# Performance work log

Measured on AMD Instinct MI355X. Metric: run time of the kernel, lower is better.

The kernel has to match this reference:

```python
import jax, jax.numpy as jnp
import numpy as np

TOTAL_WORDS = 10000
EMB = 100
SEQ = 80
UNITS = 64


def setup_inputs() -> dict:
    key = jax.random.key(0)
    ks = jax.random.split(key, 10)
    B = 16384
    tokens = jax.random.randint(ks[0], (B, SEQ), 0, TOTAL_WORDS, dtype=jnp.int32)
    s = 0.05
    emb = jax.random.normal(ks[1], (TOTAL_WORDS, EMB), jnp.float32) * s
    Wx0 = jax.random.normal(ks[2], (EMB, UNITS), jnp.float32) * s
    Wh0 = jax.random.normal(ks[3], (UNITS, UNITS), jnp.float32) * s
    b0 = jnp.zeros((UNITS,), jnp.float32)
    Wx1 = jax.random.normal(ks[4], (UNITS, UNITS), jnp.float32) * s
    Wh1 = jax.random.normal(ks[5], (UNITS, UNITS), jnp.float32) * s
    b1 = jnp.zeros((UNITS,), jnp.float32)
    Wout = jax.random.normal(ks[6], (UNITS, 1), jnp.float32) * s
    bout = jnp.zeros((1,), jnp.float32)
    return {"tokens": tokens, "emb": emb, "Wx0": Wx0, "Wh0": Wh0, "b0": b0,
            "Wx1": Wx1, "Wh1": Wh1, "b1": b1, "Wout": Wout, "bout": bout}


def reference(tokens, emb, Wx0, Wh0, b0, Wx1, Wh1, b1, Wout, bout):
    # Embedding lookup: [B, SEQ, EMB]
    x = emb[tokens]
    B = tokens.shape[0]
    # time-major for scan: [SEQ, B, EMB]
    xt = jnp.transpose(x, (1, 0, 2))
    h0 = jnp.zeros((B, UNITS), x.dtype)
    h1 = jnp.zeros((B, UNITS), x.dtype)

    def step(carry, x_t):
        h0, h1 = carry
        # SimpleRNNCell (inference, dropout inactive): h' = tanh(x Wx + h Wh + b)
        h0n = jnp.tanh(x_t @ Wx0 + h0 @ Wh0 + b0)
        h1n = jnp.tanh(h0n @ Wx1 + h1 @ Wh1 + b1)
        return (h0n, h1n), None

    (h0, h1), _ = jax.lax.scan(step, (h0, h1), xt)
    logits = h1 @ Wout + bout  # [B, 1]
    return jax.nn.sigmoid(logits)
```

## Files before the change

### kernel.cpp

```cpp
#include <hip/hip_runtime.h>

#define TOTAL_WORDS 10000
#define EMB 100
#define SEQ 80
#define UNITS 64
#define BATCH 16384


typedef _Float16 f16x4 __attribute__((ext_vector_type(4)));
typedef _Float16 f16x8 __attribute__((ext_vector_type(8)));
typedef _Float16 h2    __attribute__((ext_vector_type(2)));
typedef __fp16   fp16x2r __attribute__((ext_vector_type(2)));
typedef float    f32x4 __attribute__((ext_vector_type(4)));

__device__ __forceinline__ h2 pkcvt(float a, float b) {
    fp16x2r t = __builtin_amdgcn_cvt_pkrtz(a, b);
    h2 o; o[0] = (_Float16)t[0]; o[1] = (_Float16)t[1];
    return o;
}

__device__ __forceinline__ h2 tanh_h2(h2 x) {
    const _Float16 c3 = (_Float16)(-0.33333333f);
    const _Float16 c5 = (_Float16)(0.13333333f);
    h2 x2 = x * x;
    h2 p  = x2 * c5 + c3;
    h2 x3 = x2 * x;
    return x3 * p + x;
}

__device__ __forceinline__ f16x4 tanh_pack(f32x4 a) {
    h2 lo = tanh_h2(pkcvt(a[0], a[1]));
    h2 hi = tanh_h2(pkcvt(a[2], a[3]));
    f16x4 o;
    o[0] = lo[0]; o[1] = lo[1]; o[2] = hi[0]; o[3] = hi[1];
    return o;
}

__device__ __forceinline__ void lds_barrier() {
    asm volatile("s_waitcnt lgkmcnt(0)\n\ts_barrier" ::: "memory");
}

__global__ void prep_kernel(const float* __restrict__ emb,
                            const float* __restrict__ Wx0,
                            const float* __restrict__ b0,
                            const float* __restrict__ Wh0,
                            const float* __restrict__ Wx1,
                            const float* __restrict__ Wh1,
                            float* __restrict__ embW,
                            _Float16* __restrict__ wfrags) {
    int b = blockIdx.x;
    if (b < 250) {
        __shared__ float wx[EMB * UNITS];
        for (int i = threadIdx.x; i < EMB * UNITS; i += 256)
            wx[i] = Wx0[i];
        __syncthreads();
        const int u = threadIdx.x & 63;
        const int wvi = threadIdx.x >> 6;
        const int vbase = b * 40 + wvi * 10;
        const float bias = b0[u];
        float acc[10];
#pragma unroll
        for (int i = 0; i < 10; ++i) acc[i] = bias;
        const float* er = emb + vbase * EMB;
#pragma unroll 4
        for (int k = 0; k < EMB; ++k) {
            float wxv = wx[k * UNITS + u];
#pragma unroll
            for (int i = 0; i < 10; ++i)
                acc[i] = fmaf(er[i * EMB + k], wxv, acc[i]);
        }
#pragma unroll
        for (int i = 0; i < 10; ++i)
            embW[(vbase + i) * UNITS + u] = acc[i];
    } else {
        int e = (b - 250) * 256 + threadIdx.x;
        int mat = e >> 12;
        int ee = e & 4095;
        int f = ee >> 9;
        int mt = f >> 1, kf = f & 1;
        int rr = ee & 511;
        int l = rr >> 3, j = rr & 7;
        int k = kf * 32 + (l >> 4) * 8 + j;
        int col = mt * 16 + (l & 15);
        const float* W = (mat == 0) ? Wh0 : (mat == 1) ? Wx1 : Wh1;
        wfrags[e] = (_Float16)W[k * UNITS + col];
    }
}

#define RNN_STEP(EA, EB, T4)                                                  \
    {                                                                         \
        f32x4 a0 = EA, a1 = EB;               \
        f32x4 c0 = b1v0, c1 = b1v1;                  \
        a0 = __builtin_amdgcn_mfma_f32_16x16x32_f16(w0[0][0], h0f0, a0,0,0,0);\
        a1 = __builtin_amdgcn_mfma_f32_16x16x32_f16(w0[1][0], h0f0, a1,0,0,0);\
        c0 = __builtin_amdgcn_mfma_f32_16x16x32_f16(wh[0][0], h1f0, c0,0,0,0);\
        c1 = __builtin_amdgcn_mfma_f32_16x16x32_f16(wh[1][0], h1f0, c1,0,0,0);\
        a0 = __builtin_amdgcn_mfma_f32_16x16x32_f16(w0[0][1], h0f1, a0,0,0,0);\
        a1 = __builtin_amdgcn_mfma_f32_16x16x32_f16(w0[1][1], h0f1, a1,0,0,0);\
        c0 = __builtin_amdgcn_mfma_f32_16x16x32_f16(wh[0][1], h1f1, c0,0,0,0);\
        c1 = __builtin_amdgcn_mfma_f32_16x16x32_f16(wh[1][1], h1f1, c1,0,0,0);\
        EA = embWv[(T4) * 16 + (2 * p) * 4 + q];          \
        EB = embWv[(T4) * 16 + (2 * p + 1) * 4 + q];                          \
        {                                                                     \
            f16x4 n0 = tanh_pack(a0), n1 = tanh_pack(a1);                     \
            *(uint2*)&hbuf0[r][(2 * p) * 16 + 4 * q] = *(const uint2*)&n0;    \
            *(uint2*)&hbuf0[r][(2 * p + 1) * 16 + 4 * q] = *(const uint2*)&n1;\
        }                                                                     \
        lds_barrier();                                                        \
        h0f0 = *(const f16x8*)&hbuf0[r][8 * q];                               \
        h0f1 = *(const f16x8*)&hbuf0[r][32 + 8 * q];                          \
        c0 = __builtin_amdgcn_mfma_f32_16x16x32_f16(wx[0][0], h0f0, c0,0,0,0);\
        c1 = __builtin_amdgcn_mfma_f32_16x16x32_f16(wx[1][0], h0f0, c1,0,0,0);\
        c0 = __builtin_amdgcn_mfma_f32_16x16x32_f16(wx[0][1], h0f1, c0,0,0,0);\
        c1 = __builtin_amdgcn_mfma_f32_16x16x32_f16(wx[1][1], h0f1, c1,0,0,0);\
        {                                                                     \
            f16x4 n0 = tanh_pack(c0), n1 = tanh_pack(c1);                     \
            *(uint2*)&hbuf1[r][(2 * p) * 16 + 4 * q] = *(const uint2*)&n0;    \
            *(uint2*)&hbuf1[r][(2 * p + 1) * 16 + 4 * q] = *(const uint2*)&n1;\
        }                                                                     \
        lds_barrier();                                                        \
        h1f0 = *(const f16x8*)&hbuf1[r][8 * q];                               \
        h1f1 = *(const f16x8*)&hbuf1[r][32 + 8 * q];                          \
    }

__global__ __launch_bounds__(128, 2) void rnn_mfma_kernel(
    const int*      __restrict__ tokens,
    const float*    __restrict__ embW,
    const _Float16* __restrict__ wfrags,
    const float*    __restrict__ b1,
    const float*    __restrict__ Wout,
    const float*    __restrict__ bout,
    float*          __restrict__ out) {
    const int tid = threadIdx.x;
    const int p   = tid >> 6;
    const int l   = tid & 63;
    const int r   = l & 15;
    const int q   = l >> 4;
    const int row0 = blockIdx.x * 16;

    __shared__ __align__(16) _Float16 hbuf0[16][72];
    __shared__ __align__(16) _Float16 hbuf1[16][72];

    const f16x8* wf8 = (const f16x8*)wfrags;
    f16x8 w0[2][2], wx[2][2], wh[2][2];
#pragma unroll
    for (int j = 0; j < 2; ++j)
#pragma unroll
        for (int kf = 0; kf < 2; ++kf) {
            int mt = 2 * p + j;
            w0[j][kf] = wf8[(mt * 2 + kf) * 64 + l];
            wx[j][kf] = wf8[(8 + mt * 2 + kf) * 64 + l];
            wh[j][kf] = wf8[(16 + mt * 2 + kf) * 64 + l];
        }

    const f32x4 b1v0 = ((const f32x4*)b1)[(2 * p) * 4 + q];
    const f32x4 b1v1 = ((const f32x4*)b1)[(2 * p + 1) * 4 + q];

    f16x8 h0f0, h0f1, h1f0, h1f1;
#pragma unroll
    for (int j = 0; j < 8; ++j) {
        h0f0[j] = (_Float16)0.0f; h0f1[j] = (_Float16)0.0f;
        h1f0[j] = (_Float16)0.0f; h1f1[j] = (_Float16)0.0f;
    }

    const f32x4* embWv = (const f32x4*)embW;
    const int tokbase = (row0 + r) * SEQ;

    int4 tk0 = *(const int4*)&tokens[tokbase];
    int4 tk  = *(const int4*)&tokens[tokbase + 4];
    f32x4 e0a = embWv[tk0.x * 16 + (2 * p) * 4 + q];
    f32x4 e0b = embWv[tk0.x * 16 + (2 * p + 1) * 4 + q];
    f32x4 e1a = embWv[tk0.y * 16 + (2 * p) * 4 + q];
    f32x4 e1b = embWv[tk0.y * 16 + (2 * p + 1) * 4 + q];
    f32x4 e2a = embWv[tk0.z * 16 + (2 * p) * 4 + q];
    f32x4 e2b = embWv[tk0.z * 16 + (2 * p + 1) * 4 + q];
    f32x4 e3a = embWv[tk0.w * 16 + (2 * p) * 4 + q];
    f32x4 e3b = embWv[tk0.w * 16 + (2 * p + 1) * 4 + q];

    for (int k = 0; k < SEQ / 4; ++k) {
        int off = (4 * k + 8 <= SEQ - 4) ? (4 * k + 8) : (SEQ - 4);
        int4 tkC = *(const int4*)&tokens[tokbase + off];

        RNN_STEP(e0a, e0b, tk.x)
        RNN_STEP(e1a, e1b, tk.y)
        RNN_STEP(e2a, e2b, tk.z)
        RNN_STEP(e3a, e3b, tk.w)

        tk = tkC;
    }

    if (p == 0) {
        f32x4 wo0 = ((const f32x4*)Wout)[2 * q];
        f32x4 wo1 = ((const f32x4*)Wout)[2 * q + 1];
        f32x4 wo2 = ((const f32x4*)Wout)[8 + 2 * q];
        f32x4 wo3 = ((const f32x4*)Wout)[8 + 2 * q + 1];
        float accv = 0.0f;
#pragma unroll
        for (int j = 0; j < 4; ++j) {
            accv = fmaf((float)h1f0[j],     wo0[j], accv);
            accv = fmaf((float)h1f0[4 + j], wo1[j], accv);
            accv = fmaf((float)h1f1[j],     wo2[j], accv);
            accv = fmaf((float)h1f1[4 + j], wo3[j], accv);
        }
        accv += __shfl_down(accv, 16);
        accv += __shfl_down(accv, 32);
        if (l < 16) {
            float z = accv + bout[0];
            out[row0 + r] = 1.0f / (1.0f + __expf(-z));
        }
    }
}

extern "C" void kernel_launch(void* const* d_in, const int* in_sizes, int n_in,
                              void* d_out, int out_size, void* d_ws, size_t ws_size,
                              hipStream_t stream) {
    const int*   tokens = (const int*)d_in[0];
    const float* emb    = (const float*)d_in[1];
    const float* Wx0    = (const float*)d_in[2];
    const float* Wh0    = (const float*)d_in[3];
    const float* b0     = (const float*)d_in[4];
    const float* Wx1    = (const float*)d_in[5];
    const float* Wh1    = (const float*)d_in[6];
    const float* b1     = (const float*)d_in[7];
    const float* Wout   = (const float*)d_in[8];
    const float* bout   = (const float*)d_in[9];
    float* out = (float*)d_out;

    float* embW = (float*)d_ws;
    _Float16* wfrags =
        (_Float16*)((char*)d_ws + (size_t)TOTAL_WORDS * UNITS * 4);

    prep_kernel<<<298, 256, 0, stream>>>(emb, Wx0, b0, Wh0, Wx1, Wh1,
                                         embW, wfrags);
    rnn_mfma_kernel<<<BATCH / 16, 128, 0, stream>>>(tokens, embW, wfrags,
                                                    b1, Wout, bout, out);
}
```

Before: 130.7 us.

## Split RNN units across four waves and process two 16-row tiles per block

Each block now has four waves that each own one 16-unit M tile, and handles 32 batch rows as two independent 16-row tiles instead of one. Every wave issues two independent MFMA chains per substep, one per row tile, so fewer weight fragments stay resident and each wave has more independent work to hide MFMA and tanh latency. The embedding prefetch distance drops from four steps to two, and the barriers now synchronise four waves instead of two, so barrier cost and exposed gather latency may rise.

Result: slower. 134.3 us (+2.7%).

```diff
diff --git a/kernel.cpp b/kernel.cpp
--- a/kernel.cpp
+++ b/kernel.cpp
@@ -39,6 +39,8 @@
 __device__ __forceinline__ void lds_barrier() {
     asm volatile("s_waitcnt lgkmcnt(0)\n\ts_barrier" ::: "memory");
 }
+
+#define M32(W, H, C) __builtin_amdgcn_mfma_f32_16x16x32_f16((W), (H), (C), 0, 0, 0)
 
 __global__ void prep_kernel(const float* __restrict__ emb,
                             const float* __restrict__ Wx0,
@@ -87,43 +89,44 @@
     }
 }
 
-#define RNN_STEP(EA, EB, T4)                                                  \
+#define SUBSTEP(E0, E1, T20, T21)                                             \
     {                                                                         \
-        f32x4 a0 = EA, a1 = EB;               \
-        f32x4 c0 = b1v0, c1 = b1v1;                  \
-        a0 = __builtin_amdgcn_mfma_f32_16x16x32_f16(w0[0][0], h0f0, a0,0,0,0);\
-        a1 = __builtin_amdgcn_mfma_f32_16x16x32_f16(w0[1][0], h0f0, a1,0,0,0);\
-        c0 = __builtin_amdgcn_mfma_f32_16x16x32_f16(wh[0][0], h1f0, c0,0,0,0);\
-        c1 = __builtin_amdgcn_mfma_f32_16x16x32_f16(wh[1][0], h1f0, c1,0,0,0);\
-        a0 = __builtin_amdgcn_mfma_f32_16x16x32_f16(w0[0][1], h0f1, a0,0,0,0);\
-        a1 = __builtin_amdgcn_mfma_f32_16x16x32_f16(w0[1][1], h0f1, a1,0,0,0);\
-        c0 = __builtin_amdgcn_mfma_f32_16x16x32_f16(wh[0][1], h1f1, c0,0,0,0);\
-        c1 = __builtin_amdgcn_mfma_f32_16x16x32_f16(wh[1][1], h1f1, c1,0,0,0);\
-        EA = embWv[(T4) * 16 + (2 * p) * 4 + q];          \
-        EB = embWv[(T4) * 16 + (2 * p + 1) * 4 + q];                          \
+        f32x4 a0 = E0, a1 = E1;                                               \
+        f32x4 c0 = b1v, c1 = b1v;                                             \
+                          \
+        a0 = M32(w0f[0], h0A0, a0);  a1 = M32(w0f[0], h0A1, a1);              \
+        c0 = M32(whf[0], h1A0, c0);  c1 = M32(whf[0], h1A1, c1);              \
+        a0 = M32(w0f[1], h0B0, a0);  a1 = M32(w0f[1], h0B1, a1);              \
+        c0 = M32(whf[1], h1B0, c0);  c1 = M32(whf[1], h1B1, c1);              \
         {                                                                     \
             f16x4 n0 = tanh_pack(a0), n1 = tanh_pack(a1);                     \
-            *(uint2*)&hbuf0[r][(2 * p) * 16 + 4 * q] = *(const uint2*)&n0;    \
-            *(uint2*)&hbuf0[r][(2 * p + 1) * 16 + 4 * q] = *(const uint2*)&n1;\
+            *(uint2*)&hbuf0[0][r][p * 16 + 4 * q] = *(const uint2*)&n0;       \
+            *(uint2*)&hbuf0[1][r][p * 16 + 4 * q] = *(const uint2*)&n1;       \
         }                                                                     \
         lds_barrier();                                                        \
-        h0f0 = *(const f16x8*)&hbuf0[r][8 * q];                               \
-        h0f1 = *(const f16x8*)&hbuf0[r][32 + 8 * q];                          \
-        c0 = __builtin_amdgcn_mfma_f32_16x16x32_f16(wx[0][0], h0f0, c0,0,0,0);\
-        c1 = __builtin_amdgcn_mfma_f32_16x16x32_f16(wx[1][0], h0f0, c1,0,0,0);\
-        c0 = __builtin_amdgcn_mfma_f32_16x16x32_f16(wx[0][1], h0f1, c0,0,0,0);\
-        c1 = __builtin_amdgcn_mfma_f32_16x16x32_f16(wx[1][1], h0f1, c1,0,0,0);\
+        h0A0 = *(const f16x8*)&hbuf0[0][r][8 * q];                            \
+        h0B0 = *(const f16x8*)&hbuf0[0][r][32 + 8 * q];                       \
+        h0A1 = *(const f16x8*)&hbuf0[1][r][8 * q];                            \
+        h0B1 = *(const f16x8*)&hbuf0[1][r][32 + 8 * q];                       \
+                      \
+        E0 = embWv[(T20) * 16 + p * 4 + q];                                   \
+        E1 = embWv[(T21) * 16 + p * 4 + q];                                   \
+                            \
+        c0 = M32(wxf[0], h0A0, c0);  c1 = M32(wxf[0], h0A1, c1);              \
+        c0 = M32(wxf[1], h0B0, c0);  c1 = M32(wxf[1], h0B1, c1);              \
         {                                                                     \
             f16x4 n0 = tanh_pack(c0), n1 = tanh_pack(c1);                     \
-            *(uint2*)&hbuf1[r][(2 * p) * 16 + 4 * q] = *(const uint2*)&n0;    \
-            *(uint2*)&hbuf1[r][(2 * p + 1) * 16 + 4 * q] = *(const uint2*)&n1;\
+            *(uint2*)&hbuf1[0][r][p * 16 + 4 * q] = *(const uint2*)&n0;       \
+            *(uint2*)&hbuf1[1][r][p * 16 + 4 * q] = *(const uint2*)&n1;       \
         }                                                                     \
         lds_barrier();                                                        \
-        h1f0 = *(const f16x8*)&hbuf1[r][8 * q];                               \
-        h1f1 = *(const f16x8*)&hbuf1[r][32 + 8 * q];                          \
-    }
-
-__global__ __launch_bounds__(128, 2) void rnn_mfma_kernel(
+        h1A0 = *(const f16x8*)&hbuf1[0][r][8 * q];                            \
+        h1B0 = *(const f16x8*)&hbuf1[0][r][32 + 8 * q];                       \
+        h1A1 = *(const f16x8*)&hbuf1[1][r][8 * q];                            \
+        h1B1 = *(const f16x8*)&hbuf1[1][r][32 + 8 * q];                       \
+    }
+
+__global__ __launch_bounds__(256, 2) void rnn_mfma_kernel(
     const int*      __restrict__ tokens,
     const float*    __restrict__ embW,
     const _Float16* __restrict__ wfrags,
@@ -136,57 +139,53 @@
     const int l   = tid & 63;
     const int r   = l & 15;
     const int q   = l >> 4;
-    const int row0 = blockIdx.x * 16;
-
-    __shared__ __align__(16) _Float16 hbuf0[16][72];
-    __shared__ __align__(16) _Float16 hbuf1[16][72];
+    const int row0 = blockIdx.x * 32;
+
+    __shared__ __align__(16) _Float16 hbuf0[2][16][72];
+    __shared__ __align__(16) _Float16 hbuf1[2][16][72];
 
     const f16x8* wf8 = (const f16x8*)wfrags;
-    f16x8 w0[2][2], wx[2][2], wh[2][2];
-#pragma unroll
-    for (int j = 0; j < 2; ++j)
-#pragma unroll
-        for (int kf = 0; kf < 2; ++kf) {
-            int mt = 2 * p + j;
-            w0[j][kf] = wf8[(mt * 2 + kf) * 64 + l];
-            wx[j][kf] = wf8[(8 + mt * 2 + kf) * 64 + l];
-            wh[j][kf] = wf8[(16 + mt * 2 + kf) * 64 + l];
-        }
-
-    const f32x4 b1v0 = ((const f32x4*)b1)[(2 * p) * 4 + q];
-    const f32x4 b1v1 = ((const f32x4*)b1)[(2 * p + 1) * 4 + q];
-
-    f16x8 h0f0, h0f1, h1f0, h1f1;
+    f16x8 w0f[2], wxf[2], whf[2];
+#pragma unroll
+    for (int kf = 0; kf < 2; ++kf) {
+        w0f[kf] = wf8[(p * 2 + kf) * 64 + l];
+        wxf[kf] = wf8[(8 + p * 2 + kf) * 64 + l];
+        whf[kf] = wf8[(16 + p * 2 + kf) * 64 + l];
+    }
+    const f32x4 b1v = ((const f32x4*)b1)[p * 4 + q];
+
+    f16x8 h0A0, h0B0, h1A0, h1B0;
+    f16x8 h0A1, h0B1, h1A1, h1B1;
 #pragma unroll
     for (int j = 0; j < 8; ++j) {
-        h0f0[j] = (_Float16)0.0f; h0f1[j] = (_Float16)0.0f;
-        h1f0[j] = (_Float16)0.0f; h1f1[j] = (_Float16)0.0f;
+        h0A0[j] = (_Float16)0.0f; h0B0[j] = (_Float16)0.0f;
+        h1A0[j] = (_Float16)0.0f; h1B0[j] = (_Float16)0.0f;
+        h0A1[j] = (_Float16)0.0f; h0B1[j] = (_Float16)0.0f;
+        h1A1[j] = (_Float16)0.0f; h1B1[j] = (_Float16)0.0f;
     }
 
     const f32x4* embWv = (const f32x4*)embW;
-    const int tokbase = (row0 + r) * SEQ;
-
-    int4 tk0 = *(const int4*)&tokens[tokbase];
-    int4 tk  = *(const int4*)&tokens[tokbase + 4];
-    f32x4 e0a = embWv[tk0.x * 16 + (2 * p) * 4 + q];
-    f32x4 e0b = embWv[tk0.x * 16 + (2 * p + 1) * 4 + q];
-    f32x4 e1a = embWv[tk0.y * 16 + (2 * p) * 4 + q];
-    f32x4 e1b = embWv[tk0.y * 16 + (2 * p + 1) * 4 + q];
-    f32x4 e2a = embWv[tk0.z * 16 + (2 * p) * 4 + q];
-    f32x4 e2b = embWv[tk0.z * 16 + (2 * p + 1) * 4 + q];
-    f32x4 e3a = embWv[tk0.w * 16 + (2 * p) * 4 + q];
-    f32x4 e3b = embWv[tk0.w * 16 + (2 * p + 1) * 4 + q];
+    const int tokbase0 = (row0 + r) * SEQ;
+    const int tokbase1 = (row0 + 16 + r) * SEQ;
+
+    int4 tk0 = *(const int4*)&tokens[tokbase0];
+    int4 tk1 = *(const int4*)&tokens[tokbase1];
+    f32x4 e00 = embWv[tk0.x * 16 + p * 4 + q];
+    f32x4 e01 = embWv[tk0.y * 16 + p * 4 + q];
+    f32x4 e10 = embWv[tk1.x * 16 + p * 4 + q];
+    f32x4 e11 = embWv[tk1.y * 16 + p * 4 + q];
 
     for (int k = 0; k < SEQ / 4; ++k) {
-        int off = (4 * k + 8 <= SEQ - 4) ? (4 * k + 8) : (SEQ - 4);
-        int4 tkC = *(const int4*)&tokens[tokbase + off];
-
-        RNN_STEP(e0a, e0b, tk.x)
-        RNN_STEP(e1a, e1b, tk.y)
-        RNN_STEP(e2a, e2b, tk.z)
-        RNN_STEP(e3a, e3b, tk.w)
-
-        tk = tkC;
+        int off = (4 * k + 4 <= SEQ - 4) ? (4 * k + 4) : (SEQ - 4);
+        int4 tkN0 = *(const int4*)&tokens[tokbase0 + off];
+        int4 tkN1 = *(const int4*)&tokens[tokbase1 + off];
+
+        SUBSTEP(e00, e10, tk0.z, tk1.z)
+        SUBSTEP(e01, e11, tk0.w, tk1.w)
+        SUBSTEP(e00, e10, tkN0.x, tkN1.x)
+        SUBSTEP(e01, e11, tkN0.y, tkN1.y)
+
+        tk0 = tkN0; tk1 = tkN1;
     }
 
     if (p == 0) {
@@ -194,19 +193,25 @@
         f32x4 wo1 = ((const f32x4*)Wout)[2 * q + 1];
         f32x4 wo2 = ((const f32x4*)Wout)[8 + 2 * q];
         f32x4 wo3 = ((const f32x4*)Wout)[8 + 2 * q + 1];
-        float accv = 0.0f;
+        float acc0 = 0.0f, acc1 = 0.0f;
 #pragma unroll
         for (int j = 0; j < 4; ++j) {
-            accv = fmaf((float)h1f0[j],     wo0[j], accv);
-            accv = fmaf((float)h1f0[4 + j], wo1[j], accv);
-            accv = fmaf((float)h1f1[j],     wo2[j], accv);
-            accv = fmaf((float)h1f1[4 + j], wo3[j], accv);
+            acc0 = fmaf((float)h1A0[j],     wo0[j], acc0);
+            acc0 = fmaf((float)h1A0[4 + j], wo1[j], acc0);
+            acc0 = fmaf((float)h1B0[j],     wo2[j], acc0);
+            acc0 = fmaf((float)h1B0[4 + j], wo3[j], acc0);
+            acc1 = fmaf((float)h1A1[j],     wo0[j], acc1);
+            acc1 = fmaf((float)h1A1[4 + j], wo1[j], acc1);
+            acc1 = fmaf((float)h1B1[j],     wo2[j], acc1);
+            acc1 = fmaf((float)h1B1[4 + j], wo3[j], acc1);
         }
-        accv += __shfl_down(accv, 16);
-        accv += __shfl_down(accv, 32);
+        acc0 += __shfl_down(acc0, 16);
+        acc0 += __shfl_down(acc0, 32);
+        acc1 += __shfl_down(acc1, 16);
+        acc1 += __shfl_down(acc1, 32);
         if (l < 16) {
-            float z = accv + bout[0];
-            out[row0 + r] = 1.0f / (1.0f + __expf(-z));
+            out[row0 + r]      = 1.0f / (1.0f + __expf(-(acc0 + bout[0])));
+            out[row0 + 16 + r] = 1.0f / (1.0f + __expf(-(acc1 + bout[0])));
         }
     }
 }
@@ -232,6 +237,6 @@
 
     prep_kernel<<<298, 256, 0, stream>>>(emb, Wx0, b0, Wh0, Wx1, Wh1,
                                          embW, wfrags);
-    rnn_mfma_kernel<<<BATCH / 16, 128, 0, stream>>>(tokens, embW, wfrags,
+    rnn_mfma_kernel<<<BATCH / 32, 256, 0, stream>>>(tokens, embW, wfrags,
                                                     b1, Wout, bout, out);
 }
```
